# Optimization experiments

Measured on AMD Instinct MI355X. Metric: run time of the kernel, lower is better.

## Reference

```python
import jax, jax.numpy as jnp
import numpy as np

MAX_TRIES = 50
EPS = 1e-38  # fp32-safe stand-in for torch's 1e-40 clamps


def _l2norm(x, axis=-1):
    n = jnp.sqrt(jnp.sum(x * x, axis=axis, keepdims=True))
    return x / jnp.maximum(n, 1e-12)


def _wood_sample_vmf(key, mu, kappa):
    """Vectorized Wood's algorithm vMF sampling. mu: [B,d] unit vectors, kappa: [B]."""
    B, d = mu.shape
    alpha = d - 1.0

    def step(carry, i):
        w, acc = carry
        k1, k2 = jax.random.split(jax.random.fold_in(key, i))
        w_cand = 2.0 * jax.random.uniform(k1, (B,)) - 1.0
        one_minus_w2 = jnp.clip(1.0 - w_cand * w_cand, EPS, None)
        log_p = kappa * w_cand + 0.5 * (alpha - 2.0) * jnp.log(one_minus_w2)
        log_r = jnp.log(jax.random.uniform(k2, (B,)) + EPS)
        new = (log_r + kappa <= log_p) & (~acc)
        w = jnp.where(new, w_cand, w)
        return (w, acc | new), None

    (w, _), _ = jax.lax.scan(step, (jnp.zeros((B,)), jnp.zeros((B,), bool)),
                             jnp.arange(MAX_TRIES))
    w = jnp.clip(w, -1.0, 1.0)

    kv = jax.random.fold_in(key, 10_000)
    v = _l2norm(jax.random.normal(kv, (B, d - 1)))          # uniform on S^{d-2}
    sqrt_term = jnp.sqrt(jnp.clip(1.0 - w * w, EPS, None))
    z_tilde = jnp.concatenate([sqrt_term[:, None] * v, w[:, None]], axis=-1)  # [B,d]

    e_d = jnp.zeros((d,)).at[-1].set(1.0)
    u = _l2norm(e_d[None, :] - mu)                           # Householder axis
    dot_val = jnp.sum(z_tilde * u, axis=-1, keepdims=True)
    return z_tilde - 2.0 * dot_val * u


def reference(h, W_mu, b_mu, W_k, b_k, W1, b1, W2, b2, W3, b3, seed):
    # encode (h = flattened resnet features [B, 512])
    mu = _l2norm(h @ W_mu.T + b_mu)                          # [B, latent]
    kappa = jax.nn.softplus(h @ W_k.T + b_k) + 1.0           # [B, 1]
    # reparameterize via Wood's algorithm
    key = jax.random.key(seed)
    z = _wood_sample_vmf(key, mu, kappa[:, 0])               # [B, latent]
    # MLP head: latent -> 512 -> 32 -> num_classes*action_length
    x = jax.nn.relu(z @ W1.T + b1)
    x = jax.nn.relu(x @ W2.T + b2)
    out = x @ W3.T + b3                                      # [B, 7]
    return out, mu, kappa


def setup_inputs() -> dict:
    key = jax.random.key(0)
    ks = jax.random.split(key, 8)
    B, F, L, H, Ffin, O = 131072, 512, 32, 512, 32, 7
    s = lambda fan_in: 1.0 / np.sqrt(fan_in)
    return {
        "h":    jax.random.normal(ks[0], (B, F), jnp.float32),
        "W_mu": jax.random.uniform(ks[1], (L, F), jnp.float32, -s(F), s(F)),
        "b_mu": jnp.zeros((L,), jnp.float32),
        "W_k":  jax.random.uniform(ks[2], (1, F), jnp.float32, -s(F), s(F)),
        "b_k":  jnp.zeros((1,), jnp.float32),
        "W1":   jax.random.uniform(ks[3], (H, L), jnp.float32, -s(L), s(L)),
        "b1":   jnp.zeros((H,), jnp.float32),
        "W2":   jax.random.uniform(ks[4], (Ffin, H), jnp.float32, -s(H), s(H)),
        "b2":   jnp.zeros((Ffin,), jnp.float32),
        "W3":   jax.random.uniform(ks[5], (O, Ffin), jnp.float32, -s(Ffin), s(Ffin)),
        "b3":   jnp.zeros((O,), jnp.float32),
        "seed": 0,
    }
```

## Files before the change

### kernel.cpp

```cpp
#include <hip/hip_runtime.h>
#include <hip/hip_bf16.h>
#include <math.h>
#include <stdint.h>

#define NTRY  50
#define BROWS 131072
#define OFF_OUT_MU    917504
#define OFF_OUT_KAPPA 5111808

__device__ __forceinline__ uint32_t rotl32(uint32_t x, int r){ return (x << r) | (x >> (32 - r)); }

__device__ __forceinline__ void threefry2x32(uint32_t k0, uint32_t k1,
                                             uint32_t c0, uint32_t c1,
                                             uint32_t& o0, uint32_t& o1){
  const uint32_t k2 = k0 ^ k1 ^ 0x1BD11BDAu;
  uint32_t x0 = c0 + k0;
  uint32_t x1 = c1 + k1;
#define TF_R(r) { x0 += x1; x1 = rotl32(x1, (r)); x1 ^= x0; }
  TF_R(13) TF_R(15) TF_R(26) TF_R(6)
  x0 += k1; x1 += k2 + 1u;
  TF_R(17) TF_R(29) TF_R(16) TF_R(24)
  x0 += k2; x1 += k0 + 2u;
  TF_R(13) TF_R(15) TF_R(26) TF_R(6)
  x0 += k0; x1 += k1 + 3u;
  TF_R(17) TF_R(29) TF_R(16) TF_R(24)
  x0 += k1; x1 += k2 + 4u;
  TF_R(13) TF_R(15) TF_R(26) TF_R(6)
  x0 += k2; x1 += k0 + 5u;
#undef TF_R
  o0 = x0; o1 = x1;
}

__device__ __forceinline__ uint32_t tf_bits32(uint32_t k0, uint32_t k1, uint32_t idx){
  uint32_t a, b;
  threefry2x32(k0, k1, 0u, idx, a, b);
  return a ^ b;
}

__device__ __forceinline__ float bits_to_unit(uint32_t bits){
  return __uint_as_float((bits >> 9) | 0x3f800000u) - 1.0f;
}

__device__ __forceinline__ float alogf(float x){
  return (float)log((double)x);
}

__device__ __forceinline__ float erfinv_f(float x){
  float w = -log1pf(-x * x);
  float p;
  if (w < 5.0f){
    w -= 2.5f;
    p = 2.81022636e-08f;
    p = fmaf(p, w, 3.43273939e-07f);
    p = fmaf(p, w, -3.5233877e-06f);
    p = fmaf(p, w, -4.39150654e-06f);
    p = fmaf(p, w, 0.00021858087f);
    p = fmaf(p, w, -0.00125372503f);
    p = fmaf(p, w, -0.00417768164f);
    p = fmaf(p, w, 0.246640727f);
    p = fmaf(p, w, 1.50140941f);
  } else {
    w = sqrtf(w) - 3.0f;
    p = -0.000200214257f;
    p = fmaf(p, w, 0.000100950558f);
    p = fmaf(p, w, 0.00134934322f);
    p = fmaf(p, w, -0.00367342844f);
    p = fmaf(p, w, 0.00573950773f);
    p = fmaf(p, w, -0.0076224613f);
    p = fmaf(p, w, 0.00943887047f);
    p = fmaf(p, w, 1.00167406f);
    p = fmaf(p, w, 2.83297682f);
  }
  return p * x;
}

__global__ void prep_kernel(const float* __restrict__ W2, const int* __restrict__ seedp,
                            uint32_t* __restrict__ keys, float* __restrict__ W2T)
{
  const int t = threadIdx.x;
  if (blockIdx.x == 0){
    const uint32_t seed = (uint32_t)seedp[0];
    if (t < NTRY){
      uint32_t f0, f1, a0, a1, b0, b1;
      threefry2x32(0u, seed, 0u, (uint32_t)t, f0, f1);
      threefry2x32(f0, f1, 0u, 0u, a0, a1);
      threefry2x32(f0, f1, 0u, 1u, b0, b1);
      keys[t*4+0] = a0;
      keys[t*4+1] = a1;
      keys[t*4+2] = b0;
      keys[t*4+3] = b1;
    } else if (t == NTRY){
      uint32_t f0, f1;
      threefry2x32(0u, seed, 0u, 10000u, f0, f1);
      keys[200] = f0; keys[201] = f1;
    }
  }
  const int j = blockIdx.x * 256 + t;
  const int o1 = j >> 5, o2 = j & 31;
  W2T[j] = W2[o2*512 + o1];
}

__global__ __launch_bounds__(512, 2) void fused_kernel(
    const float* __restrict__ h,
    const float* __restrict__ Wmu, const float* __restrict__ bmu,
    const float* __restrict__ Wk,  const float* __restrict__ bk,
    const float* __restrict__ W1,  const float* __restrict__ b1,
    const float* __restrict__ b2,
    const float* __restrict__ W3,  const float* __restrict__ b3,
    const float* __restrict__ W2T,
    const uint32_t* __restrict__ keys,
    float* __restrict__ out)
{
  __shared__ __align__(16) float lds[8192];
  const int tid = threadIdx.x;
  const int b = blockIdx.x * 512 + tid;

  const float4* h4 = reinterpret_cast<const float4*>(h + (size_t)b * 512);

  float4 hbuf[8];
  #pragma unroll
  for (int q = 0; q < 8; ++q) hbuf[q] = h4[q];

  {
    const float4* Wmu4 = reinterpret_cast<const float4*>(Wmu);
    float4* lds4 = reinterpret_cast<float4*>(lds);
    #pragma unroll
    for (int q = 0; q < 4; ++q){
      lds4[tid + q*512] = Wmu4[tid + q*512];
    }
  }
  __syncthreads();

  float acc[33];
  #pragma unroll
  for (int o = 0; o < 33; ++o) acc[o] = 0.0f;
  #pragma unroll 1
  for (int ch = 0; ch < 16; ++ch){
    float hv[32];
    #pragma unroll
    for (int q = 0; q < 8; ++q){
      float4 f = hbuf[q];
      hv[q*4+0] = f.x; hv[q*4+1] = f.y; hv[q*4+2] = f.z; hv[q*4+3] = f.w;
    }
    if (ch < 15){
      #pragma unroll
      for (int q = 0; q < 8; ++q) hbuf[q] = h4[(ch+1)*8 + q];
    }
    #pragma unroll
    for (int o = 0; o < 33; ++o){
      float a = acc[o];
      if (o < 16){
        const float4* wr4 = reinterpret_cast<const float4*>(&lds[o*512 + ch*32]);
        #pragma unroll
        for (int q = 0; q < 8; ++q){
          float4 wq = wr4[q];
          a += hv[q*4+0] * wq.x;
          a += hv[q*4+1] * wq.y;
          a += hv[q*4+2] * wq.z;
          a += hv[q*4+3] * wq.w;
        }
      } else {
        const float* wr = (o < 32) ? (Wmu + o*512 + ch*32) : (Wk + ch*32);
        #pragma unroll
        for (int c = 0; c < 32; ++c) a += hv[c] * wr[c];
      }
      acc[o] = a;
    }
  }

  float mu[32]; float nsq = 0.0f;
  #pragma unroll
  for (int o = 0; o < 32; ++o){ float m = acc[o] + bmu[o]; mu[o] = m; nsq += m*m; }
  const float invn = 1.0f / fmaxf(sqrtf(nsq), 1e-12f);
  #pragma unroll
  for (int o = 0; o < 32; ++o) mu[o] *= invn;

  const float xk = acc[32] + bk[0];
  const float kappa = (float)log1p(exp((double)xk)) + 1.0f;

  {
    float4* mo = reinterpret_cast<float4*>(out + OFF_OUT_MU + (size_t)b * 32);
    #pragma unroll
    for (int q = 0; q < 8; ++q){
      float4 f; f.x = mu[q*4+0]; f.y = mu[q*4+1]; f.z = mu[q*4+2]; f.w = mu[q*4+3];
      mo[q] = f;
    }
    out[OFF_OUT_KAPPA + b] = kappa;
  }

  __syncthreads();
  {
    const float4* W2T_4 = reinterpret_cast<const float4*>(W2T);
    float4 tmp[4];
    #pragma unroll
    for (int q = 0; q < 4; ++q){
      tmp[q] = W2T_4[tid + q*512];
    }
    float4* lds4 = reinterpret_cast<float4*>(lds);
    #pragma unroll
    for (int q = 0; q < 4; ++q){
      lds4[tid + q*512] = tmp[q];
    }
  }

  const uint32_t ub = (uint32_t)b;

  float w = 0.0f; bool done = false;
  #pragma unroll 2
  for (int i = 0; i < NTRY; ++i){
    #pragma clang fp contract(off)
    const uint32_t K0 = keys[i*4+0], K1 = keys[i*4+1];
    const uint32_t K2 = keys[i*4+2], K3 = keys[i*4+3];
    const float u1 = bits_to_unit(tf_bits32(K0, K1, ub));
    const float u2 = bits_to_unit(tf_bits32(K2, K3, ub));
    const float wc   = 2.0f * u1 - 1.0f;
    const float ww   = wc * wc;
    const float omw2 = fmaxf(1.0f - ww, 1e-38f);
    const float lg   = alogf(omw2);
    const float lp   = kappa * wc + 14.5f * lg;
    const float lr   = alogf(u2 + 1e-38f);
    const bool  cnd  = (lr + kappa <= lp) && !done;
    if (cnd){ w = wc; done = true; }
    if (__all(done)) break;
  }
  w = fminf(fmaxf(w, -1.0f), 1.0f);

  const uint32_t kv0 = keys[200], kv1 = keys[201];
  float v[31]; float vns = 0.0f;
  const uint32_t e0 = ub * 31u;
  #pragma unroll
  for (int j = 0; j < 31; ++j){
    const float uf01 = bits_to_unit(tf_bits32(kv0, kv1, e0 + (uint32_t)j));
    const float u = fmaxf(uf01 * 2.0f + (-0.99999994f), -0.99999994f);
    const float g = 1.4142135623730951f * erfinv_f(u);
    v[j] = g; vns += g * g;
  }
  const float invvn = 1.0f / fmaxf(sqrtf(vns), 1e-12f);
  const float st = sqrtf(fmaxf(1.0f - w * w, 1e-38f));

  float zt[32];
  #pragma unroll
  for (int j = 0; j < 31; ++j) zt[j] = st * (v[j] * invvn);
  zt[31] = w;

  float ue[32]; float uns = 0.0f;
  #pragma unroll
  for (int o = 0; o < 32; ++o){
    float e = ((o == 31) ? 1.0f : 0.0f) - mu[o];
    ue[o] = e; uns += e * e;
  }
  const float invun = 1.0f / fmaxf(sqrtf(uns), 1e-12f);
  float dot = 0.0f;
  #pragma unroll
  for (int o = 0; o < 32; ++o){ ue[o] *= invun; dot += zt[o] * ue[o]; }
  float z[32];
  #pragma unroll
  for (int o = 0; o < 32; ++o) z[o] = zt[o] - 2.0f * dot * ue[o];

  __syncthreads();
  float x2a[32];
  #pragma unroll
  for (int o2 = 0; o2 < 32; ++o2) x2a[o2] = b2[o2];
  #pragma unroll 2
  for (int o1 = 0; o1 < 256; ++o1){
    const float* w1r = W1 + o1*32;
    float t = b1[o1];
    #pragma unroll
    for (int j = 0; j < 32; ++j) t += z[j] * w1r[j];
    t = fmaxf(t, 0.0f);
    const float4* w2r4 = reinterpret_cast<const float4*>(&lds[o1*32]);
    #pragma unroll
    for (int q = 0; q < 8; ++q){
      float4 w2q = w2r4[q];
      x2a[q*4+0] += t * w2q.x;
      x2a[q*4+1] += t * w2q.y;
      x2a[q*4+2] += t * w2q.z;
      x2a[q*4+3] += t * w2q.w;
    }
  }
  #pragma unroll 2
  for (int o1 = 256; o1 < 512; ++o1){
    const float* w1r = W1 + o1*32;
    float t = b1[o1];
    #pragma unroll
    for (int j = 0; j < 32; ++j) t += z[j] * w1r[j];
    t = fmaxf(t, 0.0f);
    const float* w2r = W2T + o1*32;
    #pragma unroll
    for (int o2 = 0; o2 < 32; ++o2) x2a[o2] += t * w2r[o2];
  }
  #pragma unroll
  for (int o2 = 0; o2 < 32; ++o2) x2a[o2] = fmaxf(x2a[o2], 0.0f);

  float* orow = out + (size_t)b * 7;
  #pragma unroll
  for (int k = 0; k < 7; ++k){
    const float* w3r = W3 + k*32;
    float s = b3[k];
    #pragma unroll
    for (int o2 = 0; o2 < 32; ++o2) s += x2a[o2] * w3r[o2];
    orow[k] = s;
  }
}

extern "C" void kernel_launch(void* const* d_in, const int* in_sizes, int n_in,
                              void* d_out, int out_size, void* d_ws, size_t ws_size,
                              hipStream_t stream)
{
  const float* h   = (const float*)d_in[0];
  const float* Wmu = (const float*)d_in[1];
  const float* bmu = (const float*)d_in[2];
  const float* Wk  = (const float*)d_in[3];
  const float* bk  = (const float*)d_in[4];
  const float* W1  = (const float*)d_in[5];
  const float* b1  = (const float*)d_in[6];
  const float* W2  = (const float*)d_in[7];
  const float* b2  = (const float*)d_in[8];
  const float* W3  = (const float*)d_in[9];
  const float* b3  = (const float*)d_in[10];
  const int* seed  = (const int*)d_in[11];

  uint32_t* keys = (uint32_t*)d_ws;
  float* W2T = (float*)((char*)d_ws + 1024);
  float* out = (float*)d_out;

  hipLaunchKernelGGL(prep_kernel, dim3(64), dim3(256), 0, stream, W2, seed, keys, W2T);
  hipLaunchKernelGGL(fused_kernel, dim3(BROWS/512), dim3(512), 0, stream,
                     h, Wmu, bmu, Wk, bk, W1, b1, b2, W3, b3, W2T, keys, out);
}
```

Measured before the change: 747.5 us.

## Split each row across two threads with role-based work division

Each row is now handled by two threads instead of one. One thread computes half of the mu projection, and the other computes the other half plus kappa, with partial sums exchanged through LDS. The rejection sampling and the Gaussian direction generation run on different threads. The W2 product is split by output halves, and W2 is transposed into lo/hi halves. This is meant to cut per-thread register pressure and serial latency and to raise occupancy (launch bounds 512,4). The cost is twice as many h loads (both threads read the full row), recomputing the W1 layer in both threads, extra syncs, and an LDS footprint that may limit blocks per CU.

```diff
diff --git a/kernel.cpp b/kernel.cpp
--- a/kernel.cpp
+++ b/kernel.cpp
@@ -75,7 +75,8 @@
 }
 
 __global__ void prep_kernel(const float* __restrict__ W2, const int* __restrict__ seedp,
-                            uint32_t* __restrict__ keys, float* __restrict__ W2T)
+                            uint32_t* __restrict__ keys, float* __restrict__ W2Tlo,
+                            float* __restrict__ W2Thi)
 {
   const int t = threadIdx.x;
   if (blockIdx.x == 0){
@@ -97,23 +98,28 @@
   }
   const int j = blockIdx.x * 256 + t;
   const int o1 = j >> 5, o2 = j & 31;
-  W2T[j] = W2[o2*512 + o1];
-}
-
-__global__ __launch_bounds__(512, 2) void fused_kernel(
+  const float val = W2[o2*512 + o1];
+  if (o2 < 16) W2Tlo[o1*16 + o2]      = val;
+  else         W2Thi[o1*16 + (o2-16)] = val;
+}
+
+__global__ __launch_bounds__(512, 4) void fused_kernel(
     const float* __restrict__ h,
     const float* __restrict__ Wmu, const float* __restrict__ bmu,
     const float* __restrict__ Wk,  const float* __restrict__ bk,
     const float* __restrict__ W1,  const float* __restrict__ b1,
     const float* __restrict__ b2,
     const float* __restrict__ W3,  const float* __restrict__ b3,
-    const float* __restrict__ W2T,
+    const float* __restrict__ W2Tlo, const float* __restrict__ W2Thi,
     const uint32_t* __restrict__ keys,
     float* __restrict__ out)
 {
-  __shared__ __align__(16) float lds[8192];
+  __shared__ __align__(16) float lds[16640];
   const int tid = threadIdx.x;
-  const int b = blockIdx.x * 512 + tid;
+  const int rlocal = tid & 255;
+  const int role = tid >> 8;
+  const int b = blockIdx.x * 256 + rlocal;
+  float* exch = &lds[8192 + rlocal * 33];
 
   const float4* h4 = reinterpret_cast<const float4*>(h + (size_t)b * 512);
 
@@ -125,15 +131,13 @@
     const float4* Wmu4 = reinterpret_cast<const float4*>(Wmu);
     float4* lds4 = reinterpret_cast<float4*>(lds);
     #pragma unroll
-    for (int q = 0; q < 4; ++q){
-      lds4[tid + q*512] = Wmu4[tid + q*512];
-    }
-  }
-  __syncthreads();
-
-  float acc[33];
-  #pragma unroll
-  for (int o = 0; o < 33; ++o) acc[o] = 0.0f;
+    for (int q = 0; q < 4; ++q) lds4[tid + q*512] = Wmu4[tid + q*512];
+  }
+  __syncthreads();
+
+  float acc[17];
+  #pragma unroll
+  for (int i = 0; i < 17; ++i) acc[i] = 0.0f;
   #pragma unroll 1
   for (int ch = 0; ch < 16; ++ch){
     float hv[32];
@@ -146,11 +150,11 @@
       #pragma unroll
       for (int q = 0; q < 8; ++q) hbuf[q] = h4[(ch+1)*8 + q];
     }
-    #pragma unroll
-    for (int o = 0; o < 33; ++o){
-      float a = acc[o];
-      if (o < 16){
+    if (role == 0){
+      #pragma unroll
+      for (int o = 0; o < 16; ++o){
         const float4* wr4 = reinterpret_cast<const float4*>(&lds[o*512 + ch*32]);
+        float a = acc[o];
         #pragma unroll
         for (int q = 0; q < 8; ++q){
           float4 wq = wr4[q];
@@ -159,26 +163,55 @@
           a += hv[q*4+2] * wq.z;
           a += hv[q*4+3] * wq.w;
         }
-      } else {
+        acc[o] = a;
+      }
+    } else {
+      #pragma unroll
+      for (int i = 0; i < 17; ++i){
+        const int o = 16 + i;
         const float* wr = (o < 32) ? (Wmu + o*512 + ch*32) : (Wk + ch*32);
+        float a = acc[i];
         #pragma unroll
         for (int c = 0; c < 32; ++c) a += hv[c] * wr[c];
+        acc[i] = a;
       }
-      acc[o] = a;
-    }
-  }
+    }
+  }
+
+  if (role == 0){
+    #pragma unroll
+    for (int i = 0; i < 16; ++i) exch[i] = acc[i];
+  } else {
+    #pragma unroll
+    for (int i = 0; i < 17; ++i) exch[16 + i] = acc[i];
+  }
+  __syncthreads();
+
+  {
+    const float4* W2Tlo4 = reinterpret_cast<const float4*>(W2Tlo);
+    float4 tmp[4];
+    #pragma unroll
+    for (int q = 0; q < 4; ++q) tmp[q] = W2Tlo4[tid + q*512];
+    float4* lds4 = reinterpret_cast<float4*>(lds);
+    #pragma unroll
+    for (int q = 0; q < 4; ++q) lds4[tid + q*512] = tmp[q];
+  }
+
+  float accf[33];
+  #pragma unroll
+  for (int o = 0; o < 33; ++o) accf[o] = exch[o];
 
   float mu[32]; float nsq = 0.0f;
   #pragma unroll
-  for (int o = 0; o < 32; ++o){ float m = acc[o] + bmu[o]; mu[o] = m; nsq += m*m; }
+  for (int o = 0; o < 32; ++o){ float m = accf[o] + bmu[o]; mu[o] = m; nsq += m*m; }
   const float invn = 1.0f / fmaxf(sqrtf(nsq), 1e-12f);
   #pragma unroll
   for (int o = 0; o < 32; ++o) mu[o] *= invn;
 
-  const float xk = acc[32] + bk[0];
+  const float xk = accf[32] + bk[0];
   const float kappa = (float)log1p(exp((double)xk)) + 1.0f;
 
-  {
+  if (role == 0){
     float4* mo = reinterpret_cast<float4*>(out + OFF_OUT_MU + (size_t)b * 32);
     #pragma unroll
     for (int q = 0; q < 8; ++q){
@@ -187,57 +220,53 @@
     }
     out[OFF_OUT_KAPPA + b] = kappa;
   }
-
-  __syncthreads();
-  {
-    const float4* W2T_4 = reinterpret_cast<const float4*>(W2T);
-    float4 tmp[4];
-    #pragma unroll
-    for (int q = 0; q < 4; ++q){
-      tmp[q] = W2T_4[tid + q*512];
-    }
-    float4* lds4 = reinterpret_cast<float4*>(lds);
-    #pragma unroll
-    for (int q = 0; q < 4; ++q){
-      lds4[tid + q*512] = tmp[q];
-    }
-  }
+  __syncthreads();
 
   const uint32_t ub = (uint32_t)b;
-
-  float w = 0.0f; bool done = false;
-  #pragma unroll 2
-  for (int i = 0; i < NTRY; ++i){
-    #pragma clang fp contract(off)
-    const uint32_t K0 = keys[i*4+0], K1 = keys[i*4+1];
-    const uint32_t K2 = keys[i*4+2], K3 = keys[i*4+3];
-    const float u1 = bits_to_unit(tf_bits32(K0, K1, ub));
-    const float u2 = bits_to_unit(tf_bits32(K2, K3, ub));
-    const float wc   = 2.0f * u1 - 1.0f;
-    const float ww   = wc * wc;
-    const float omw2 = fmaxf(1.0f - ww, 1e-38f);
-    const float lg   = alogf(omw2);
-    const float lp   = kappa * wc + 14.5f * lg;
-    const float lr   = alogf(u2 + 1e-38f);
-    const bool  cnd  = (lr + kappa <= lp) && !done;
-    if (cnd){ w = wc; done = true; }
-    if (__all(done)) break;
-  }
-  w = fminf(fmaxf(w, -1.0f), 1.0f);
-
-  const uint32_t kv0 = keys[200], kv1 = keys[201];
-  float v[31]; float vns = 0.0f;
-  const uint32_t e0 = ub * 31u;
-  #pragma unroll
-  for (int j = 0; j < 31; ++j){
-    const float uf01 = bits_to_unit(tf_bits32(kv0, kv1, e0 + (uint32_t)j));
-    const float u = fmaxf(uf01 * 2.0f + (-0.99999994f), -0.99999994f);
-    const float g = 1.4142135623730951f * erfinv_f(u);
-    v[j] = g; vns += g * g;
-  }
+  if (role == 0){
+    float w = 0.0f; bool done = false;
+    #pragma unroll 2
+    for (int i = 0; i < NTRY; ++i){
+      #pragma clang fp contract(off)
+      const uint32_t K0 = keys[i*4+0], K1 = keys[i*4+1];
+      const uint32_t K2 = keys[i*4+2], K3 = keys[i*4+3];
+      const float u1 = bits_to_unit(tf_bits32(K0, K1, ub));
+      const float u2 = bits_to_unit(tf_bits32(K2, K3, ub));
+      const float wc   = 2.0f * u1 - 1.0f;
+      const float ww   = wc * wc;
+      const float omw2 = fmaxf(1.0f - ww, 1e-38f);
+      const float lg   = alogf(omw2);
+      const float lp   = kappa * wc + 14.5f * lg;
+      const float lr   = alogf(u2 + 1e-38f);
+      const bool  cnd  = (lr + kappa <= lp) && !done;
+      if (cnd){ w = wc; done = true; }
+      if (__all(done)) break;
+    }
+    w = fminf(fmaxf(w, -1.0f), 1.0f);
+    exch[32] = w;
+  } else {
+    const uint32_t kv0 = keys[200], kv1 = keys[201];
+    float vns = 0.0f;
+    const uint32_t e0 = ub * 31u;
+    #pragma unroll
+    for (int j = 0; j < 31; ++j){
+      const float uf01 = bits_to_unit(tf_bits32(kv0, kv1, e0 + (uint32_t)j));
+      const float u = fmaxf(uf01 * 2.0f + (-0.99999994f), -0.99999994f);
+      const float g = 1.4142135623730951f * erfinv_f(u);
+      exch[j] = g; vns += g * g;
+    }
+    exch[31] = vns;
+  }
+  __syncthreads();
+
+  const float w = exch[32];
+  float v[31];
+  #pragma unroll
+  for (int j = 0; j < 31; ++j) v[j] = exch[j];
+  const float vns = exch[31];
+
   const float invvn = 1.0f / fmaxf(sqrtf(vns), 1e-12f);
   const float st = sqrtf(fmaxf(1.0f - w * w, 1e-38f));
-
   float zt[32];
   #pragma unroll
   for (int j = 0; j < 31; ++j) zt[j] = st * (v[j] * invvn);
@@ -257,49 +286,61 @@
   #pragma unroll
   for (int o = 0; o < 32; ++o) z[o] = zt[o] - 2.0f * dot * ue[o];
 
-  __syncthreads();
-  float x2a[32];
-  #pragma unroll
-  for (int o2 = 0; o2 < 32; ++o2) x2a[o2] = b2[o2];
-  #pragma unroll 2
-  for (int o1 = 0; o1 < 256; ++o1){
-    const float* w1r = W1 + o1*32;
-    float t = b1[o1];
-    #pragma unroll
-    for (int j = 0; j < 32; ++j) t += z[j] * w1r[j];
-    t = fmaxf(t, 0.0f);
-    const float4* w2r4 = reinterpret_cast<const float4*>(&lds[o1*32]);
-    #pragma unroll
-    for (int q = 0; q < 8; ++q){
-      float4 w2q = w2r4[q];
-      x2a[q*4+0] += t * w2q.x;
-      x2a[q*4+1] += t * w2q.y;
-      x2a[q*4+2] += t * w2q.z;
-      x2a[q*4+3] += t * w2q.w;
-    }
-  }
-  #pragma unroll 2
-  for (int o1 = 256; o1 < 512; ++o1){
-    const float* w1r = W1 + o1*32;
-    float t = b1[o1];
-    #pragma unroll
-    for (int j = 0; j < 32; ++j) t += z[j] * w1r[j];
-    t = fmaxf(t, 0.0f);
-    const float* w2r = W2T + o1*32;
-    #pragma unroll
-    for (int o2 = 0; o2 < 32; ++o2) x2a[o2] += t * w2r[o2];
-  }
-  #pragma unroll
-  for (int o2 = 0; o2 < 32; ++o2) x2a[o2] = fmaxf(x2a[o2], 0.0f);
-
-  float* orow = out + (size_t)b * 7;
-  #pragma unroll
-  for (int k = 0; k < 7; ++k){
-    const float* w3r = W3 + k*32;
-    float s = b3[k];
-    #pragma unroll
-    for (int o2 = 0; o2 < 32; ++o2) s += x2a[o2] * w3r[o2];
-    orow[k] = s;
+  float x2a[16];
+  #pragma unroll
+  for (int k = 0; k < 16; ++k) x2a[k] = b2[role*16 + k];
+  if (role == 0){
+    #pragma unroll 2
+    for (int o1 = 0; o1 < 512; ++o1){
+      const float* w1r = W1 + o1*32;
+      float t = b1[o1];
+      #pragma unroll
+      for (int j = 0; j < 32; ++j) t += z[j] * w1r[j];
+      t = fmaxf(t, 0.0f);
+      const float4* w2r4 = reinterpret_cast<const float4*>(&lds[o1*16]);
+      #pragma unroll
+      for (int q = 0; q < 4; ++q){
+        float4 wq = w2r4[q];
+        x2a[q*4+0] += t * wq.x;
+        x2a[q*4+1] += t * wq.y;
+        x2a[q*4+2] += t * wq.z;
+        x2a[q*4+3] += t * wq.w;
+      }
+    }
+  } else {
+    #pragma unroll 2
+    for (int o1 = 0; o1 < 512; ++o1){
+      const float* w1r = W1 + o1*32;
+      float t = b1[o1];
+      #pragma unroll
+      for (int j = 0; j < 32; ++j) t += z[j] * w1r[j];
+      t = fmaxf(t, 0.0f);
+      const float* w2r = W2Thi + o1*16;
+      #pragma unroll
+      for (int k = 0; k < 16; ++k) x2a[k] += t * w2r[k];
+    }
+  }
+  __syncthreads();
+  if (role == 1){
+    #pragma unroll
+    for (int k = 0; k < 16; ++k) exch[k] = x2a[k];
+  }
+  __syncthreads();
+  if (role == 0){
+    float xf[32];
+    #pragma unroll
+    for (int k = 0; k < 16; ++k) xf[k] = fmaxf(x2a[k], 0.0f);
+    #pragma unroll
+    for (int k = 0; k < 16; ++k) xf[16 + k] = fmaxf(exch[k], 0.0f);
+    float* orow = out + (size_t)b * 7;
+    #pragma unroll
+    for (int kk = 0; kk < 7; ++kk){
+      const float* w3r = W3 + kk*32;
+      float s = b3[kk];
+      #pragma unroll
+      for (int o2 = 0; o2 < 32; ++o2) s += xf[o2] * w3r[o2];
+      orow[kk] = s;
+    }
   }
 }
 
@@ -321,10 +362,11 @@
   const int* seed  = (const int*)d_in[11];
 
   uint32_t* keys = (uint32_t*)d_ws;
-  float* W2T = (float*)((char*)d_ws + 1024);
+  float* W2Tlo = (float*)((char*)d_ws + 1024);
+  float* W2Thi = (float*)((char*)d_ws + 1024 + 32768);
   float* out = (float*)d_out;
 
-  hipLaunchKernelGGL(prep_kernel, dim3(64), dim3(256), 0, stream, W2, seed, keys, W2T);
-  hipLaunchKernelGGL(fused_kernel, dim3(BROWS/512), dim3(512), 0, stream,
-                     h, Wmu, bmu, Wk, bk, W1, b1, b2, W3, b3, W2T, keys, out);
-}
+  hipLaunchKernelGGL(prep_kernel, dim3(64), dim3(256), 0, stream, W2, seed, keys, W2Tlo, W2Thi);
+  hipLaunchKernelGGL(fused_kernel, dim3(BROWS/256), dim3(512), 0, stream,
+                     h, Wmu, bmu, Wk, bk, W1, b1, b2, W3, b3, W2Tlo, W2Thi, keys, out);
+}
```

New measurement: 739.4 us. About the same (-1.1%).
